# Kernel optimization log

Measured on AMD Instinct MI355X. Metric: run time of the kernel, lower is better.

Reference implementation:

```python
import jax, jax.numpy as jnp
import numpy as np
import math

D_MODEL = 512
N_HEADS = 8
D_K = D_MODEL // N_HEADS
B, L_Q, L_K = 4, 2048, 2048


def setup_inputs() -> dict:
    key = jax.random.key(0)
    ks = jax.random.split(key, 12)
    s = 1.0 / math.sqrt(D_MODEL)
    inp = {
        "Q_in": jax.random.normal(ks[0], (B, L_Q, D_MODEL), jnp.float32),
        "K_in": jax.random.normal(ks[1], (B, L_K, D_MODEL), jnp.float32),
        "V_in": jax.random.normal(ks[2], (B, L_K, D_MODEL), jnp.float32),
        "Wq": jax.random.normal(ks[3], (D_MODEL, D_MODEL), jnp.float32) * s,
        "bq": jnp.zeros((D_MODEL,), jnp.float32),
        "Wk": jax.random.normal(ks[4], (D_MODEL, D_MODEL), jnp.float32) * s,
        "bk": jnp.zeros((D_MODEL,), jnp.float32),
        "Wv": jax.random.normal(ks[5], (D_MODEL, D_MODEL), jnp.float32) * s,
        "bv": jnp.zeros((D_MODEL,), jnp.float32),
        "Wo": jax.random.normal(ks[6], (D_MODEL, D_MODEL), jnp.float32) * s,
        "bo": jnp.zeros((D_MODEL,), jnp.float32),
        "log_omega": jax.random.normal(ks[7], (N_HEADS, 1, 1), jnp.float32) - 2.0,
    }
    return inp


def reference(Q_in, K_in, V_in, Wq, bq, Wk, bk, Wv, bv, Wo, bo, log_omega):
    B_, Lq, _ = Q_in.shape
    Lk = K_in.shape[1]
    # projections (torch Linear: x @ W.T + b), split into heads -> [B,H,L,Dk]
    Q = (Q_in @ Wq.T + bq).reshape(B_, Lq, N_HEADS, D_K).transpose(0, 2, 1, 3)
    K = (K_in @ Wk.T + bk).reshape(B_, Lk, N_HEADS, D_K).transpose(0, 2, 1, 3)
    V = (V_in @ Wv.T + bv).reshape(B_, Lk, N_HEADS, D_K).transpose(0, 2, 1, 3)
    # raw logits [B,H,Lq,Lk]
    logits = jnp.einsum("bhqd,bhkd->bhqk", Q, K) / math.sqrt(D_K)
    # learnable cosine phase bias: cos(2*pi*omega*delta_t), omega per head
    delta_t = jnp.arange(Lq, dtype=jnp.float32)[:, None] - jnp.arange(Lk, dtype=jnp.float32)[None, :]
    omega = jnp.exp(log_omega)  # [H,1,1]
    phase_bias = jnp.cos(2.0 * math.pi * omega * delta_t[None])  # [H,Lq,Lk]
    logits = logits + phase_bias[None]
    attn = jax.nn.softmax(logits, axis=-1)  # dropout = identity (eval mode)
    out = jnp.einsum("bhqk,bhkd->bhqd", attn, V)
    out = out.transpose(0, 2, 1, 3).reshape(B_, Lq, D_MODEL)
    return out @ Wo.T + bo, attn
```

## Files before the change

kernel.cpp:

```cpp
#include <hip/hip_runtime.h>
#include <math.h>


#define DEV __device__ __forceinline__

using f32x4 = __attribute__((ext_vector_type(4))) float;
using s16x8 = __attribute__((ext_vector_type(8))) short;
using s16x4 = __attribute__((ext_vector_type(4))) short;

constexpr int NB_ = 4;
constexpr int NH_ = 8;
constexpr int L_  = 2048;
constexpr int DM_ = 512;
constexpr int DK_ = 64;

DEV short f2bf(float f) {
  unsigned u = __float_as_uint(f);
  u += 0x7fffu + ((u >> 16) & 1u);
  return (short)(u >> 16);
}
DEV float bf2f(short s) {
  return __uint_as_float((unsigned)(unsigned short)s << 16);
}
DEV f32x4 mfma16(s16x8 a, s16x8 b, f32x4 c) {
  return __builtin_amdgcn_mfma_f32_16x16x32_bf16(a, b, c, 0, 0, 0);
}
DEV void split8(const float* f, s16x8& hi, s16x8& lo) {
#pragma unroll
  for (int j = 0; j < 8; ++j) {
    short h = f2bf(f[j]);
    hi[j] = h;
    lo[j] = f2bf(f[j] - bf2f(h));
  }
}

__global__ void tab_kernel(const float* __restrict__ log_omega,
                           float* __restrict__ ctab, float* __restrict__ stab) {
  int h = blockIdx.y;
  int t = blockIdx.x * 256 + threadIdx.x;
  float om = expf(log_omega[h]);
  double a = 6.283185307179586 * (double)om * (double)t;
  ctab[h * L_ + t] = (float)cos(a);
  stab[h * L_ + t] = (float)sin(a);
}

__global__ __launch_bounds__(256, 2)
void proj_kernel(const float* __restrict__ Qin, const float* __restrict__ Kin,
                 const float* __restrict__ Vin,
                 const float* __restrict__ Wq, const float* __restrict__ bq,
                 const float* __restrict__ Wk, const float* __restrict__ bk,
                 const float* __restrict__ Wv, const float* __restrict__ bv,
                 short* __restrict__ Qh, short* __restrict__ Ql,
                 short* __restrict__ Kh, short* __restrict__ Kl,
                 short* __restrict__ Vt) {
  __shared__ short Ash[128 * 32], Asl[128 * 32], Bsh[128 * 32], Bsl[128 * 32];
  const int z = blockIdx.z;
  const float* X = (z == 0) ? Qin : (z == 1) ? Kin : Vin;
  const float* W = (z == 0) ? Wq : (z == 1) ? Wk : Wv;
  const float* bias = (z == 0) ? bq : (z == 1) ? bk : bv;
  const int m0 = blockIdx.x * 128, n0 = blockIdx.y * 128;
  const int t = threadIdx.x, lane = t & 63, w = t >> 6;
  const int wr = w >> 1, wc = w & 1;
  const int fr = lane & 15, fg = lane >> 4;

  f32x4 acc[4][4];
#pragma unroll
  for (int a = 0; a < 4; ++a)
#pragma unroll
    for (int b = 0; b < 4; ++b) acc[a][b] = f32x4{0.f, 0.f, 0.f, 0.f};

  for (int kt = 0; kt < 16; ++kt) {
    __syncthreads();
#pragma unroll
    for (int cc = 0; cc < 2; ++cc) {
      int cid = t + cc * 256;
      int row = cid >> 2, kb = cid & 3;
      float fa[8], fb[8];
      const float* ga = X + (size_t)(m0 + row) * DM_ + kt * 32 + kb * 8;
      const float* gb = W + (size_t)(n0 + row) * DM_ + kt * 32 + kb * 8;
      *(f32x4*)&fa[0] = *(const f32x4*)ga;  *(f32x4*)&fa[4] = *(const f32x4*)(ga + 4);
      *(f32x4*)&fb[0] = *(const f32x4*)gb;  *(f32x4*)&fb[4] = *(const f32x4*)(gb + 4);
      s16x8 hi, lo;
      split8(fa, hi, lo);
      ((s16x8*)Ash)[cid] = hi; ((s16x8*)Asl)[cid] = lo;
      split8(fb, hi, lo);
      ((s16x8*)Bsh)[cid] = hi; ((s16x8*)Bsl)[cid] = lo;
    }
    __syncthreads();
    s16x8 ah[4], al[4], bh_[4], bl_[4];
#pragma unroll
    for (int fm = 0; fm < 4; ++fm) {
      int r = wr * 64 + fm * 16 + fr;
      ah[fm] = ((const s16x8*)Ash)[r * 4 + fg];
      al[fm] = ((const s16x8*)Asl)[r * 4 + fg];
    }
#pragma unroll
    for (int fn = 0; fn < 4; ++fn) {
      int r = wc * 64 + fn * 16 + fr;
      bh_[fn] = ((const s16x8*)Bsh)[r * 4 + fg];
      bl_[fn] = ((const s16x8*)Bsl)[r * 4 + fg];
    }
#pragma unroll
    for (int fm = 0; fm < 4; ++fm)
#pragma unroll
      for (int fn = 0; fn < 4; ++fn) {
        acc[fm][fn] = mfma16(ah[fm], bh_[fn], acc[fm][fn]);
        acc[fm][fn] = mfma16(ah[fm], bl_[fn], acc[fm][fn]);
        acc[fm][fn] = mfma16(al[fm], bh_[fn], acc[fm][fn]);
      }
  }

  const float scale = (z == 0) ? 0.125f : 1.0f;
#pragma unroll
  for (int fn = 0; fn < 4; ++fn) {
    int C = n0 + wc * 64 + fn * 16 + fr;
    float bb = bias[C];
    int hh = C >> 6, d = C & 63;
#pragma unroll
    for (int fm = 0; fm < 4; ++fm) {
      int Rbase = m0 + wr * 64 + fm * 16 + fg * 4;
      if (z < 2) {
        short* Dh = (z == 0) ? Qh : Kh;
        short* Dl = (z == 0) ? Ql : Kl;
#pragma unroll
        for (int i = 0; i < 4; ++i) {
          int R = Rbase + i;
          int b = R >> 11, lq = R & 2047;
          float v = (acc[fm][fn][i] + bb) * scale;
          short h16 = f2bf(v);
          size_t off = ((size_t)(b * NH_ + hh) * L_ + lq) * DK_ + d;
          Dh[off] = h16;
          Dl[off] = f2bf(v - bf2f(h16));
        }
      } else {
        s16x4 p;
#pragma unroll
        for (int i = 0; i < 4; ++i) p[i] = f2bf(acc[fm][fn][i] + bb);
        int b = Rbase >> 11, lq = Rbase & 2047;
        size_t off = ((size_t)(b * NH_ + hh) * DK_ + d) * L_ + lq;
        *(s16x4*)(Vt + off) = p;
      }
    }
  }
}

__global__ __launch_bounds__(512, 1)
void attn_kernel(const short* __restrict__ Qh, const short* __restrict__ Ql,
                 const short* __restrict__ Kh, const short* __restrict__ Kl,
                 const short* __restrict__ Vt,
                 const float* __restrict__ ctab, const float* __restrict__ stab,
                 float* __restrict__ attn, short* __restrict__ heads) {
  __shared__ short P[16 * 2048];
  const int bh = blockIdx.y, q0 = blockIdx.x * 16;
  const int b = bh >> 3, h = bh & 7;
  const int tid = threadIdx.x, w = tid >> 6, lane = tid & 63;
  const int fr = lane & 15, fg = lane >> 4;
  const int wk0 = w * 256;

  size_t qoff = ((size_t)bh * L_ + q0 + fr) * DK_ + fg * 8;
  s16x8 qh0 = *(const s16x8*)(Qh + qoff), qh1 = *(const s16x8*)(Qh + qoff + 32);
  s16x8 ql0 = *(const s16x8*)(Ql + qoff), ql1 = *(const s16x8*)(Ql + qoff + 32);
  float cq[4], sq[4];
#pragma unroll
  for (int i = 0; i < 4; ++i) {
    cq[i] = ctab[h * L_ + q0 + fg * 4 + i];
    sq[i] = stab[h * L_ + q0 + fg * 4 + i];
  }

  f32x4 S[16];
#pragma unroll
  for (int t = 0; t < 16; ++t) {
    int kr = wk0 + t * 16 + fr;
    size_t koff = ((size_t)bh * L_ + kr) * DK_ + fg * 8;
    s16x8 kh0 = *(const s16x8*)(Kh + koff), kh1 = *(const s16x8*)(Kh + koff + 32);
    s16x8 kl0 = *(const s16x8*)(Kl + koff), kl1 = *(const s16x8*)(Kl + koff + 32);
    float ck = ctab[h * L_ + kr], sk = stab[h * L_ + kr];
    f32x4 c = f32x4{0.f, 0.f, 0.f, 0.f};
    c = mfma16(qh0, kh0, c); c = mfma16(qh1, kh1, c);
    c = mfma16(qh0, kl0, c); c = mfma16(qh1, kl1, c);
    c = mfma16(ql0, kh0, c); c = mfma16(ql1, kh1, c);
#pragma unroll
    for (int i = 0; i < 4; ++i) c[i] += cq[i] * ck + sq[i] * sk;
    S[t] = c;
  }

  float m[4];
#pragma unroll
  for (int i = 0; i < 4; ++i) m[i] = -1e30f;
#pragma unroll
  for (int t = 0; t < 16; ++t)
#pragma unroll
    for (int i = 0; i < 4; ++i) m[i] = fmaxf(m[i], S[t][i]);
#pragma unroll
  for (int d = 1; d < 16; d <<= 1)
#pragma unroll
    for (int i = 0; i < 4; ++i) m[i] = fmaxf(m[i], __shfl_xor(m[i], d));
  float* sm = (float*)P;
  float* ss = sm + 128;
  if (fr == 0)
#pragma unroll
    for (int i = 0; i < 4; ++i) sm[(fg * 4 + i) * 8 + w] = m[i];
  __syncthreads();
  float gm[4], sum[4] = {0.f, 0.f, 0.f, 0.f};
#pragma unroll
  for (int i = 0; i < 4; ++i) {
    float mm = -1e30f;
#pragma unroll
    for (int ww = 0; ww < 8; ++ww) mm = fmaxf(mm, sm[(fg * 4 + i) * 8 + ww]);
    gm[i] = mm;
  }
#pragma unroll
  for (int t = 0; t < 16; ++t)
#pragma unroll
    for (int i = 0; i < 4; ++i) {
      float e = __expf(S[t][i] - gm[i]);
      S[t][i] = e;
      sum[i] += e;
    }
#pragma unroll
  for (int d = 1; d < 16; d <<= 1)
#pragma unroll
    for (int i = 0; i < 4; ++i) sum[i] += __shfl_xor(sum[i], d);
  if (fr == 0)
#pragma unroll
    for (int i = 0; i < 4; ++i) ss[(fg * 4 + i) * 8 + w] = sum[i];
  __syncthreads();
  float invl[4];
#pragma unroll
  for (int i = 0; i < 4; ++i) {
    float s_ = 0.f;
#pragma unroll
    for (int ww = 0; ww < 8; ++ww) s_ += ss[(fg * 4 + i) * 8 + ww];
    invl[i] = 1.0f / s_;
  }
  __syncthreads();

#pragma unroll
  for (int t = 0; t < 16; ++t) {
    int col = wk0 + t * 16 + fr;
#pragma unroll
    for (int i = 0; i < 4; ++i) {
      int row = fg * 4 + i;
      float p = S[t][i] * invl[i];
      attn[((size_t)bh * L_ + q0 + row) * L_ + col] = p;
      int chunk = (col >> 3) ^ (row & 7);
      P[row * 2048 + chunk * 8 + (col & 7)] = f2bf(p);
    }
  }
  __syncthreads();

  if (w < 4) {
    int d0 = w * 16;
    f32x4 o = f32x4{0.f, 0.f, 0.f, 0.f};
    size_t vbase = ((size_t)bh * DK_ + d0 + fr) * L_;
#pragma unroll 4
    for (int kt = 0; kt < 64; ++kt) {
      int swz = (kt * 4 + fg) ^ (fr & 7);
      s16x8 a = *(const s16x8*)&P[fr * 2048 + swz * 8];
      s16x8 vb = *(const s16x8*)(Vt + vbase + kt * 32 + fg * 8);
      o = mfma16(a, vb, o);
    }
#pragma unroll
    for (int i = 0; i < 4; ++i) {
      int R = q0 + fg * 4 + i;
      heads[((size_t)b * L_ + R) * DM_ + h * DK_ + d0 + fr] = f2bf(o[i]);
    }
  }
}

__global__ __launch_bounds__(256, 2)
void oproj_kernel(const short* __restrict__ A, const float* __restrict__ W,
                  const float* __restrict__ bias, float* __restrict__ out) {
  __shared__ short As[128 * 32], Bs[128 * 32];
  const int m0 = blockIdx.x * 128, n0 = blockIdx.y * 128;
  const int t = threadIdx.x, lane = t & 63, w = t >> 6;
  const int wr = w >> 1, wc = w & 1;
  const int fr = lane & 15, fg = lane >> 4;

  f32x4 acc[4][4];
#pragma unroll
  for (int a = 0; a < 4; ++a)
#pragma unroll
    for (int b = 0; b < 4; ++b) acc[a][b] = f32x4{0.f, 0.f, 0.f, 0.f};

  for (int kt = 0; kt < 16; ++kt) {
    __syncthreads();
#pragma unroll
    for (int cc = 0; cc < 2; ++cc) {
      int cid = t + cc * 256;
      int row = cid >> 2, kb = cid & 3;
      ((s16x8*)As)[cid] =
          *(const s16x8*)(A + (size_t)(m0 + row) * DM_ + kt * 32 + kb * 8);
      const float* gb = W + (size_t)(n0 + row) * DM_ + kt * 32 + kb * 8;
      float fb[8];
      *(f32x4*)&fb[0] = *(const f32x4*)gb;  *(f32x4*)&fb[4] = *(const f32x4*)(gb + 4);
      s16x8 hb;
#pragma unroll
      for (int j = 0; j < 8; ++j) hb[j] = f2bf(fb[j]);
      ((s16x8*)Bs)[cid] = hb;
    }
    __syncthreads();
    s16x8 af[4], bf[4];
#pragma unroll
    for (int fm = 0; fm < 4; ++fm)
      af[fm] = ((const s16x8*)As)[(wr * 64 + fm * 16 + fr) * 4 + fg];
#pragma unroll
    for (int fn = 0; fn < 4; ++fn)
      bf[fn] = ((const s16x8*)Bs)[(wc * 64 + fn * 16 + fr) * 4 + fg];
#pragma unroll
    for (int fm = 0; fm < 4; ++fm)
#pragma unroll
      for (int fn = 0; fn < 4; ++fn) acc[fm][fn] = mfma16(af[fm], bf[fn], acc[fm][fn]);
  }
#pragma unroll
  for (int fn = 0; fn < 4; ++fn) {
    int C = n0 + wc * 64 + fn * 16 + fr;
    float bb = bias[C];
#pragma unroll
    for (int fm = 0; fm < 4; ++fm) {
      int Rbase = m0 + wr * 64 + fm * 16 + fg * 4;
#pragma unroll
      for (int i = 0; i < 4; ++i)
        out[(size_t)(Rbase + i) * DM_ + C] = acc[fm][fn][i] + bb;
    }
  }
}

extern "C" void kernel_launch(void* const* d_in, const int* in_sizes, int n_in,
                              void* d_out, int out_size, void* d_ws, size_t ws_size,
                              hipStream_t stream) {
  const float* Qin = (const float*)d_in[0];
  const float* Kin = (const float*)d_in[1];
  const float* Vin = (const float*)d_in[2];
  const float* Wq  = (const float*)d_in[3];
  const float* bq  = (const float*)d_in[4];
  const float* Wk  = (const float*)d_in[5];
  const float* bk  = (const float*)d_in[6];
  const float* Wv  = (const float*)d_in[7];
  const float* bv  = (const float*)d_in[8];
  const float* Wo  = (const float*)d_in[9];
  const float* bo  = (const float*)d_in[10];
  const float* lw  = (const float*)d_in[11];

  char* ws = (char*)d_ws;
  const size_t SZ = (size_t)NB_ * NH_ * L_ * DK_ * 2;
  short* Qh = (short*)(ws);
  short* Ql = (short*)(ws + SZ);
  short* Kh = (short*)(ws + 2 * SZ);
  short* Kl = (short*)(ws + 3 * SZ);
  short* Vt = (short*)(ws + 4 * SZ);
  short* heads = (short*)(ws + 5 * SZ);
  float* ctab = (float*)(ws + 6 * SZ);
  float* stab = ctab + NH_ * L_;

  float* out  = (float*)d_out;
  float* attn = out + (size_t)NB_ * L_ * DM_;

  tab_kernel<<<dim3(L_ / 256, NH_), 256, 0, stream>>>(lw, ctab, stab);
  proj_kernel<<<dim3(64, 4, 3), 256, 0, stream>>>(Qin, Kin, Vin, Wq, bq, Wk, bk,
                                                  Wv, bv, Qh, Ql, Kh, Kl, Vt);
  attn_kernel<<<dim3(L_ / 16, NB_ * NH_), 512, 0, stream>>>(Qh, Ql, Kh, Kl, Vt,
                                                            ctab, stab, attn, heads);
  oproj_kernel<<<dim3(64, 4), 256, 0, stream>>>(heads, Wo, bo, out);
}
```

Before: 1.076 ms.

## Restructure attention as per-wave two-pass online softmax with XCD-aware grid mapping

Replaces the 512-thread block, which held a full 16x2048 score row across waves with cross-wave LDS reductions and a 64KB P buffer, with 256-thread blocks in which each wave owns 16 query rows. Each wave runs two streaming passes over keys: the first computes the running max and sum, the second recomputes QK^T, writes normalized probabilities to attn and accumulates PV through a small swizzled per-wave LDS tile. The grid is remapped so that blocks sharing a batch-head land on the same XCD, which is meant to improve L2 reuse of K and V. In exchange, QK^T is computed twice, and the transposed MFMA orientation gives wider vectorized attn stores. The aim is to cut LDS use and barriers and to raise occupancy.

```diff
diff --git a/kernel.cpp b/kernel.cpp
--- a/kernel.cpp
+++ b/kernel.cpp
@@ -144,127 +144,113 @@
   }
 }
 
-__global__ __launch_bounds__(512, 1)
+__global__ __launch_bounds__(256, 3)
 void attn_kernel(const short* __restrict__ Qh, const short* __restrict__ Ql,
                  const short* __restrict__ Kh, const short* __restrict__ Kl,
                  const short* __restrict__ Vt,
                  const float* __restrict__ ctab, const float* __restrict__ stab,
                  float* __restrict__ attn, short* __restrict__ heads) {
-  __shared__ short P[16 * 2048];
-  const int bh = blockIdx.y, q0 = blockIdx.x * 16;
+  __shared__ short Pb[4][16 * 32];
+  const int wgid = blockIdx.x;
+  const int xcd = wgid & 7, j = wgid >> 3;
+  const int bh = ((j >> 5) << 3) + xcd;
+  const int qg = j & 31;
+  const int w = threadIdx.x >> 6, lane = threadIdx.x & 63;
+  const int fr = lane & 15, fg = lane >> 4;
+  const int q0 = qg * 64 + w * 16;
   const int b = bh >> 3, h = bh & 7;
-  const int tid = threadIdx.x, w = tid >> 6, lane = tid & 63;
-  const int fr = lane & 15, fg = lane >> 4;
-  const int wk0 = w * 256;
-
-  size_t qoff = ((size_t)bh * L_ + q0 + fr) * DK_ + fg * 8;
-  s16x8 qh0 = *(const s16x8*)(Qh + qoff), qh1 = *(const s16x8*)(Qh + qoff + 32);
-  s16x8 ql0 = *(const s16x8*)(Ql + qoff), ql1 = *(const s16x8*)(Ql + qoff + 32);
-  float cq[4], sq[4];
-#pragma unroll
-  for (int i = 0; i < 4; ++i) {
-    cq[i] = ctab[h * L_ + q0 + fg * 4 + i];
-    sq[i] = stab[h * L_ + q0 + fg * 4 + i];
-  }
-
-  f32x4 S[16];
-#pragma unroll
-  for (int t = 0; t < 16; ++t) {
-    int kr = wk0 + t * 16 + fr;
-    size_t koff = ((size_t)bh * L_ + kr) * DK_ + fg * 8;
-    s16x8 kh0 = *(const s16x8*)(Kh + koff), kh1 = *(const s16x8*)(Kh + koff + 32);
-    s16x8 kl0 = *(const s16x8*)(Kl + koff), kl1 = *(const s16x8*)(Kl + koff + 32);
-    float ck = ctab[h * L_ + kr], sk = stab[h * L_ + kr];
+
+  const size_t qoff = ((size_t)bh * L_ + q0 + fr) * DK_ + fg * 8;
+  const s16x8 qh0 = *(const s16x8*)(Qh + qoff), qh1 = *(const s16x8*)(Qh + qoff + 32);
+  const s16x8 ql0 = *(const s16x8*)(Ql + qoff), ql1 = *(const s16x8*)(Ql + qoff + 32);
+  const float cq = ctab[h * L_ + q0 + fr], sq = stab[h * L_ + q0 + fr];
+
+  const short* Kbh = Kh + (size_t)bh * L_ * DK_;
+  const short* Kbl = Kl + (size_t)bh * L_ * DK_;
+  const short* Vbh = Vt + (size_t)bh * DK_ * L_;
+  const float* ct = ctab + h * L_;
+  const float* st = stab + h * L_;
+
+  auto qk = [&](int kc) -> f32x4 {
+    size_t ko = (size_t)(kc + fr) * DK_ + fg * 8;
+    s16x8 kh0 = *(const s16x8*)(Kbh + ko), kh1 = *(const s16x8*)(Kbh + ko + 32);
+    s16x8 kl0 = *(const s16x8*)(Kbl + ko), kl1 = *(const s16x8*)(Kbl + ko + 32);
     f32x4 c = f32x4{0.f, 0.f, 0.f, 0.f};
-    c = mfma16(qh0, kh0, c); c = mfma16(qh1, kh1, c);
-    c = mfma16(qh0, kl0, c); c = mfma16(qh1, kl1, c);
-    c = mfma16(ql0, kh0, c); c = mfma16(ql1, kh1, c);
-#pragma unroll
-    for (int i = 0; i < 4; ++i) c[i] += cq[i] * ck + sq[i] * sk;
-    S[t] = c;
-  }
-
-  float m[4];
-#pragma unroll
-  for (int i = 0; i < 4; ++i) m[i] = -1e30f;
-#pragma unroll
-  for (int t = 0; t < 16; ++t)
-#pragma unroll
-    for (int i = 0; i < 4; ++i) m[i] = fmaxf(m[i], S[t][i]);
-#pragma unroll
-  for (int d = 1; d < 16; d <<= 1)
-#pragma unroll
-    for (int i = 0; i < 4; ++i) m[i] = fmaxf(m[i], __shfl_xor(m[i], d));
-  float* sm = (float*)P;
-  float* ss = sm + 128;
-  if (fr == 0)
-#pragma unroll
-    for (int i = 0; i < 4; ++i) sm[(fg * 4 + i) * 8 + w] = m[i];
-  __syncthreads();
-  float gm[4], sum[4] = {0.f, 0.f, 0.f, 0.f};
-#pragma unroll
-  for (int i = 0; i < 4; ++i) {
-    float mm = -1e30f;
-#pragma unroll
-    for (int ww = 0; ww < 8; ++ww) mm = fmaxf(mm, sm[(fg * 4 + i) * 8 + ww]);
-    gm[i] = mm;
-  }
-#pragma unroll
-  for (int t = 0; t < 16; ++t)
+    c = mfma16(kh0, qh0, c); c = mfma16(kh1, qh1, c);
+    c = mfma16(kl0, qh0, c); c = mfma16(kl1, qh1, c);
+    c = mfma16(kh0, ql0, c); c = mfma16(kh1, ql1, c);
+    f32x4 ck = *(const f32x4*)(ct + kc + fg * 4);
+    f32x4 sk = *(const f32x4*)(st + kc + fg * 4);
+#pragma unroll
+    for (int i = 0; i < 4; ++i) c[i] += cq * ck[i] + sq * sk[i];
+    return c;
+  };
+
+  float m = -3.0e38f, l = 0.f;
+#pragma unroll 2
+  for (int kc = 0; kc < L_; kc += 32) {
+    f32x4 s0 = qk(kc), s1 = qk(kc + 16);
+    float cm = fmaxf(fmaxf(fmaxf(s0[0], s0[1]), fmaxf(s0[2], s0[3])),
+                     fmaxf(fmaxf(s1[0], s1[1]), fmaxf(s1[2], s1[3])));
+    float mn = fmaxf(m, cm);
+    float e = 0.f;
+#pragma unroll
+    for (int i = 0; i < 4; ++i) e += __expf(s0[i] - mn) + __expf(s1[i] - mn);
+    l = l * __expf(m - mn) + e;
+    m = mn;
+  }
+  {
+    float m2 = fmaxf(m, __shfl_xor(m, 16));
+    m2 = fmaxf(m2, __shfl_xor(m2, 32));
+    l *= __expf(m - m2);
+    l += __shfl_xor(l, 16);
+    l += __shfl_xor(l, 32);
+    m = m2;
+  }
+  const float invl = 1.0f / l;
+
+  short* buf = Pb[w];
+  const int sw = fr & 3;
+  const int off0 = fr * 32 + (((fg >> 1) ^ sw) * 8) + (fg & 1) * 4;
+  const int off1 = fr * 32 + (((2 + (fg >> 1)) ^ sw) * 8) + (fg & 1) * 4;
+  const int offr = fr * 32 + ((fg ^ sw) * 8);
+  f32x4 ob[4];
+#pragma unroll
+  for (int dt = 0; dt < 4; ++dt) ob[dt] = f32x4{0.f, 0.f, 0.f, 0.f};
+
+#pragma unroll 2
+  for (int kc = 0; kc < L_; kc += 32) {
+    f32x4 s0 = qk(kc), s1 = qk(kc + 16);
+    f32x4 p0, p1;
 #pragma unroll
     for (int i = 0; i < 4; ++i) {
-      float e = __expf(S[t][i] - gm[i]);
-      S[t][i] = e;
-      sum[i] += e;
-    }
-#pragma unroll
-  for (int d = 1; d < 16; d <<= 1)
-#pragma unroll
-    for (int i = 0; i < 4; ++i) sum[i] += __shfl_xor(sum[i], d);
-  if (fr == 0)
-#pragma unroll
-    for (int i = 0; i < 4; ++i) ss[(fg * 4 + i) * 8 + w] = sum[i];
-  __syncthreads();
-  float invl[4];
-#pragma unroll
-  for (int i = 0; i < 4; ++i) {
-    float s_ = 0.f;
-#pragma unroll
-    for (int ww = 0; ww < 8; ++ww) s_ += ss[(fg * 4 + i) * 8 + ww];
-    invl[i] = 1.0f / s_;
-  }
-  __syncthreads();
-
-#pragma unroll
-  for (int t = 0; t < 16; ++t) {
-    int col = wk0 + t * 16 + fr;
-#pragma unroll
-    for (int i = 0; i < 4; ++i) {
-      int row = fg * 4 + i;
-      float p = S[t][i] * invl[i];
-      attn[((size_t)bh * L_ + q0 + row) * L_ + col] = p;
-      int chunk = (col >> 3) ^ (row & 7);
-      P[row * 2048 + chunk * 8 + (col & 7)] = f2bf(p);
-    }
-  }
-  __syncthreads();
-
-  if (w < 4) {
-    int d0 = w * 16;
-    f32x4 o = f32x4{0.f, 0.f, 0.f, 0.f};
-    size_t vbase = ((size_t)bh * DK_ + d0 + fr) * L_;
-#pragma unroll 4
-    for (int kt = 0; kt < 64; ++kt) {
-      int swz = (kt * 4 + fg) ^ (fr & 7);
-      s16x8 a = *(const s16x8*)&P[fr * 2048 + swz * 8];
-      s16x8 vb = *(const s16x8*)(Vt + vbase + kt * 32 + fg * 8);
-      o = mfma16(a, vb, o);
-    }
-#pragma unroll
-    for (int i = 0; i < 4; ++i) {
-      int R = q0 + fg * 4 + i;
-      heads[((size_t)b * L_ + R) * DM_ + h * DK_ + d0 + fr] = f2bf(o[i]);
-    }
+      p0[i] = __expf(s0[i] - m) * invl;
+      p1[i] = __expf(s1[i] - m) * invl;
+    }
+    float* arow = attn + ((size_t)bh * L_ + q0 + fr) * L_ + kc + fg * 4;
+    *(f32x4*)arow = p0;
+    *(f32x4*)(arow + 16) = p1;
+    s16x4 a0, a1;
+#pragma unroll
+    for (int i = 0; i < 4; ++i) { a0[i] = f2bf(p0[i]); a1[i] = f2bf(p1[i]); }
+    *(s16x4*)(buf + off0) = a0;
+    *(s16x4*)(buf + off1) = a1;
+    s16x8 pa = *(const s16x8*)(buf + offr);
+#pragma unroll
+    for (int dt = 0; dt < 4; ++dt) {
+      const s16x8 va =
+          *(const s16x8*)(Vbh + (size_t)(dt * 16 + fr) * L_ + kc + fg * 8);
+      ob[dt] = mfma16(va, pa, ob[dt]);
+    }
+  }
+
+#pragma unroll
+  for (int dt = 0; dt < 4; ++dt) {
+    s16x4 hv;
+#pragma unroll
+    for (int i = 0; i < 4; ++i) hv[i] = f2bf(ob[dt][i]);
+    *(s16x4*)(heads + ((size_t)b * L_ + q0 + fr) * DM_ + h * DK_ + dt * 16 +
+              fg * 4) = hv;
   }
 }
 
@@ -359,7 +345,7 @@
   tab_kernel<<<dim3(L_ / 256, NH_), 256, 0, stream>>>(lw, ctab, stab);
   proj_kernel<<<dim3(64, 4, 3), 256, 0, stream>>>(Qin, Kin, Vin, Wq, bq, Wk, bk,
                                                   Wv, bv, Qh, Ql, Kh, Kl, Vt);
-  attn_kernel<<<dim3(L_ / 16, NB_ * NH_), 512, 0, stream>>>(Qh, Ql, Kh, Kl, Vt,
-                                                            ctab, stab, attn, heads);
+  attn_kernel<<<dim3(1024), 256, 0, stream>>>(Qh, Ql, Kh, Kl, Vt, ctab, stab,
+                                              attn, heads);
   oproj_kernel<<<dim3(64, 4), 256, 0, stream>>>(heads, Wo, bo, out);
 }
```

New measurement: 1.271 ms. 18.2% more time.
